# Optimization experiments

Hardware: AMD Instinct MI355X
Metric: run time of the kernel (lower is better)

## Reference

```python
import jax, jax.numpy as jnp
import numpy as np

HIDDEN = 2048
N_HEADS = 16
N_KV_HEADS = 4
HEAD_DIM = HIDDEN // N_HEADS  # 128
FFN = 4096
N_EXPERTS = 8
TOP_K = 2
T = 2048
EPS = 1e-5
ROPE_THETA = 10000.0


def setup_inputs() -> dict:
    key = jax.random.key(0)
    ks = jax.random.split(key, 10)
    s = 0.02
    q_size = N_HEADS * HEAD_DIM
    kv_size = N_KV_HEADS * HEAD_DIM
    return {
        "hidden_states": jax.random.normal(ks[0], (T, HIDDEN), jnp.float32),
        "positions": jnp.arange(T, dtype=jnp.int32),
        "norm1_w": jnp.ones((HIDDEN,), jnp.float32),
        "norm2_w": jnp.ones((HIDDEN,), jnp.float32),
        "wqkv": jax.random.normal(ks[1], (q_size + 2 * kv_size, HIDDEN), jnp.float32) * s,
        "wo": jax.random.normal(ks[2], (HIDDEN, q_size), jnp.float32) * s,
        "gate_w": jax.random.normal(ks[3], (N_EXPERTS, HIDDEN), jnp.float32) * s,
        "w1": jax.random.normal(ks[4], (N_EXPERTS, FFN, HIDDEN), jnp.float32) * s,
        "w2": jax.random.normal(ks[5], (N_EXPERTS, HIDDEN, FFN), jnp.float32) * s,
        "w3": jax.random.normal(ks[6], (N_EXPERTS, FFN, HIDDEN), jnp.float32) * s,
    }


def _rms_norm(x, w):
    var = jnp.mean(x * x, axis=-1, keepdims=True)
    return x * jax.lax.rsqrt(var + EPS) * w


def _rope(x, positions):
    # neox-style rotary: x [T, H, D], split in halves
    half = HEAD_DIM // 2
    inv_freq = 1.0 / (ROPE_THETA ** (jnp.arange(0, half, dtype=jnp.float32) * 2.0 / HEAD_DIM))
    ang = positions.astype(jnp.float32)[:, None] * inv_freq[None, :]  # [T, half]
    cos = jnp.cos(ang)[:, None, :]  # [T, 1, half]
    sin = jnp.sin(ang)[:, None, :]
    x1, x2 = x[..., :half], x[..., half:]
    return jnp.concatenate([x1 * cos - x2 * sin, x2 * cos + x1 * sin], axis=-1)


def reference(hidden_states, positions, norm1_w, norm2_w, wqkv, wo, gate_w, w1, w2, w3):
    q_size = N_HEADS * HEAD_DIM
    kv_size = N_KV_HEADS * HEAD_DIM

    # --- input RMSNorm + attention ---
    residual = hidden_states
    h = _rms_norm(hidden_states, norm1_w)
    qkv = h @ wqkv.T  # [T, q+2kv]
    q = qkv[:, :q_size].reshape(T, N_HEADS, HEAD_DIM)
    k = qkv[:, q_size:q_size + kv_size].reshape(T, N_KV_HEADS, HEAD_DIM)
    v = qkv[:, q_size + kv_size:].reshape(T, N_KV_HEADS, HEAD_DIM)
    q = _rope(q, positions)
    k = _rope(k, positions)
    rep = N_HEADS // N_KV_HEADS
    k = jnp.repeat(k, rep, axis=1)  # [T, H, D]
    v = jnp.repeat(v, rep, axis=1)

    scale = HEAD_DIM ** -0.5
    scores = jnp.einsum('thd,shd->hts', q, k) * scale  # [H, T, T]
    causal = jnp.tril(jnp.ones((T, T), dtype=bool))
    scores = jnp.where(causal[None], scores, jnp.finfo(scores.dtype).min)
    probs = jax.nn.softmax(scores, axis=-1)
    attn = jnp.einsum('hts,shd->thd', probs, v).reshape(T, q_size)
    attn_out = attn @ wo.T

    # --- residual, post-attn RMSNorm ---
    h = attn_out + residual
    residual2 = h
    h = _rms_norm(h, norm2_w)

    # --- MoE: gate -> softmax -> top-k -> renormalize -> SwiGLU experts ---
    logits = h @ gate_w.T  # [T, E]
    routing = jax.nn.softmax(logits.astype(jnp.float32), axis=-1)
    top_vals, top_idx = jax.lax.top_k(routing, TOP_K)  # [T, K]
    top_vals = top_vals / jnp.sum(top_vals, axis=-1, keepdims=True)
    # dense per-token expert weight matrix [T, E] (zero for unselected experts)
    w_full = jnp.zeros((T, N_EXPERTS), jnp.float32).at[
        jnp.arange(T)[:, None], top_idx].add(top_vals)

    h1 = jnp.einsum('td,efd->etf', h, w1)  # [E, T, F]
    h3 = jnp.einsum('td,efd->etf', h, w3)
    g = jax.nn.silu(h1) * h3
    out_e = jnp.einsum('etf,edf->etd', g, w2)  # [E, T, D]
    moe_out = jnp.einsum('etd,te->td', out_e, w_full)

    return moe_out + residual2
```

## Files before the change

### kernel.cpp

```cpp
#include <hip/hip_runtime.h>
#include <math.h>

typedef __fp16 f16;
typedef __fp16 f16x8 __attribute__((ext_vector_type(8)));
typedef __fp16 f16x4 __attribute__((ext_vector_type(4)));
typedef float  f32x4 __attribute__((ext_vector_type(4)));

#define T_SEQ 2048
#define HID   2048
#define NQH   16
#define NKV   4
#define HD    128
#define FFN_D 4096
#define NEXP  8

#define GLDS(gp, lp) __builtin_amdgcn_global_load_lds( \
    (const __attribute__((address_space(1))) void*)(gp), \
    (__attribute__((address_space(3))) void*)(lp), 16, 0, 0)

__device__ __forceinline__ float wredsum(float v){
#pragma unroll
  for (int m = 32; m; m >>= 1) v += __shfl_xor(v, m, 64);
  return v;
}
__device__ __forceinline__ float wredmax(float v){
#pragma unroll
  for (int m = 32; m; m >>= 1) v = fmaxf(v, __shfl_xor(v, m, 64));
  return v;
}

template<bool GATHER_A>
__global__ __launch_bounds__(256, 2)
void gemm_ffn(const f16* __restrict__ A, const f16* __restrict__ B1,
              const f16* __restrict__ B3, f16* __restrict__ G,
              int K, int lda, int ldb, int ldg, long sBz,
              const int* __restrict__ grp_off, const int* __restrict__ a_rows)
{
  __shared__ __align__(16) f16 Lds[2][12288];
  const int bn = blockIdx.x, bm = blockIdx.y, e = blockIdx.z;
  const int rowBase  = grp_off[e];
  const int rowCount = grp_off[e + 1] - rowBase;
  if (rowCount <= 0 || bm * 128 >= rowCount) return;
  const f16* B1z = B1 + (long)e * sBz;
  const f16* B3z = B3 + (long)e * sBz;
  const int nt = K >> 5;

  const int tid = threadIdx.x, lane = tid & 63, w = tid >> 6;
  const int wr = w >> 1, wc = w & 1;

  const int srow = tid >> 2;
  const int scol = (((tid & 3) ^ ((tid >> 3) & 3)) << 3);
  int aoff[2], boff[2];
#pragma unroll
  for (int i = 0; i < 2; i++) {
    int r = bm * 128 + i * 64 + srow;
    if (r > rowCount - 1) r = rowCount - 1;
    const int ar = GATHER_A ? a_rows[rowBase + r] : (rowBase + r);
    aoff[i] = ar * lda + scol;
    boff[i] = (bn * 128 + i * 64 + srow) * ldb + scol;
  }

#define STGF(buf, kk) do { f16* _l = &Lds[buf][0]; \
  GLDS(A   + aoff[0] + (kk), _l +         w * 512); \
  GLDS(A   + aoff[1] + (kk), _l +  2048 + w * 512); \
  GLDS(B1z + boff[0] + (kk), _l +  4096 + w * 512); \
  GLDS(B1z + boff[1] + (kk), _l +  6144 + w * 512); \
  GLDS(B3z + boff[0] + (kk), _l +  8192 + w * 512); \
  GLDS(B3z + boff[1] + (kk), _l + 10240 + w * 512); } while (0)

  const int fr = lane & 15, fq = lane >> 4;
  const int cp = ((fq ^ ((fr >> 1) & 3)) << 3);
  const int aRow  = (wr * 64 + fr) * 32;
  const int b1Row = 4096 + (wc * 64 + fr) * 32;
  const int b3Row = 8192 + (wc * 64 + fr) * 32;

  f32x4 acc1[4][4] = {};
  f32x4 acc3[4][4] = {};

  STGF(0, 0);
  if (nt > 1) STGF(1, 32);

  for (int kt = 0; kt < nt; kt++) {
    if (kt + 1 < nt) asm volatile("s_waitcnt vmcnt(6)" ::: "memory");
    else             asm volatile("s_waitcnt vmcnt(0)" ::: "memory");
    __builtin_amdgcn_s_barrier();
    const f16* Lb = &Lds[kt & 1][0];
    f16x8 af[4], b1f[4], b3f[4];
#pragma unroll
    for (int m = 0; m < 4; m++) af[m]  = *(const f16x8*)(Lb + aRow  + m * 512 + cp);
#pragma unroll
    for (int n = 0; n < 4; n++) b1f[n] = *(const f16x8*)(Lb + b1Row + n * 512 + cp);
#pragma unroll
    for (int n = 0; n < 4; n++) b3f[n] = *(const f16x8*)(Lb + b3Row + n * 512 + cp);
    asm volatile("s_waitcnt lgkmcnt(0)" ::: "memory");
    __builtin_amdgcn_sched_barrier(0);
    __builtin_amdgcn_s_barrier();
    if (kt + 2 < nt) STGF(kt & 1, (kt + 2) * 32);
    __builtin_amdgcn_s_setprio(1);
#pragma unroll
    for (int m = 0; m < 4; m++)
#pragma unroll
      for (int n = 0; n < 4; n++) {
        acc1[m][n] = __builtin_amdgcn_mfma_f32_16x16x32_f16(af[m], b1f[n], acc1[m][n], 0, 0, 0);
        acc3[m][n] = __builtin_amdgcn_mfma_f32_16x16x32_f16(af[m], b3f[n], acc3[m][n], 0, 0, 0);
      }
    __builtin_amdgcn_s_setprio(0);
  }
#undef STGF

  const int ccol0 = bn * 128 + wc * 64 + fr;
#pragma unroll
  for (int m = 0; m < 4; m++) {
#pragma unroll
    for (int r = 0; r < 4; r++) {
      const int g = bm * 128 + wr * 64 + m * 16 + fq * 4 + r;
      if (g >= rowCount) continue;
      const long orow = rowBase + g;
#pragma unroll
      for (int n = 0; n < 4; n++) {
        const float h1 = acc1[m][n][r];
        const float h3 = acc3[m][n][r];
        const float s  = h1 / (1.0f + __expf(-h1));
        G[orow * ldg + (ccol0 + n * 16)] = (f16)(s * h3);
      }
    }
  }
}

template<bool GATHER_A, bool SCATTER_C, int EPI, int MODE>
__global__ __launch_bounds__(256, 4)
void gemm8(const f16* __restrict__ A, const f16* __restrict__ B,
           void* __restrict__ Cv, void* __restrict__ Cv2,
           int K, int lda, int ldb, int ldc, long sBz,
           const int* __restrict__ grp_off, const int* __restrict__ a_rows,
           const int* __restrict__ c_rows, const float* __restrict__ tw)
{
  __shared__ __align__(16) f16 Lds[2][8192];
  const int bn = blockIdx.x, bm = blockIdx.y, z = blockIdx.z;
  int e = z, half = 0;
  if (MODE == 1) { e = z >> 1; half = z & 1; }
  const int rowBase  = grp_off[e];
  const int rowCount = grp_off[e + 1] - rowBase;
  if (rowCount <= 0 || bm * 128 >= rowCount) return;
  const f16* Bz = B + (long)e * sBz;
  int k0 = 0, kN = K;
  if (MODE == 1) { kN = K >> 1; k0 = half * kN; }
  const int nt = kN >> 5;

  const int tid = threadIdx.x, lane = tid & 63, w = tid >> 6;
  const int wr = w >> 1, wc = w & 1;

  const int srow = tid >> 2;
  const int scol = (((tid & 3) ^ ((tid >> 3) & 3)) << 3);
  int aoff[2], boff[2];
#pragma unroll
  for (int i = 0; i < 2; i++) {
    int r = bm * 128 + i * 64 + srow;
    if (r > rowCount - 1) r = rowCount - 1;
    const int ar = GATHER_A ? a_rows[rowBase + r] : (rowBase + r);
    aoff[i] = ar * lda + scol + k0;
    boff[i] = (bn * 128 + i * 64 + srow) * ldb + scol + k0;
  }

#define STG8(buf, kk) do { f16* _l = &Lds[buf][0]; \
  GLDS(A  + aoff[0] + (kk), _l +        w * 512); \
  GLDS(A  + aoff[1] + (kk), _l + 2048 + w * 512); \
  GLDS(Bz + boff[0] + (kk), _l + 4096 + w * 512); \
  GLDS(Bz + boff[1] + (kk), _l + 6144 + w * 512); } while (0)

  const int fr = lane & 15, fq = lane >> 4;
  const int cp = ((fq ^ ((fr >> 1) & 3)) << 3);
  const int aRow = (wr * 64 + fr) * 32;
  const int bRow = 4096 + (wc * 64 + fr) * 32;

  f32x4 acc[4][4] = {};

  STG8(0, 0);
  if (nt > 1) STG8(1, 32);

  for (int kt = 0; kt < nt; kt++) {
    if (kt + 1 < nt) asm volatile("s_waitcnt vmcnt(4)" ::: "memory");
    else             asm volatile("s_waitcnt vmcnt(0)" ::: "memory");
    __builtin_amdgcn_s_barrier();
    const f16* Lb = &Lds[kt & 1][0];
    f16x8 bf[4], af[4];
#pragma unroll
    for (int n = 0; n < 4; n++) bf[n] = *(const f16x8*)(Lb + bRow + n * 512 + cp);
#pragma unroll
    for (int m = 0; m < 4; m++) af[m] = *(const f16x8*)(Lb + aRow + m * 512 + cp);
    asm volatile("s_waitcnt lgkmcnt(0)" ::: "memory");
    __builtin_amdgcn_sched_barrier(0);
    __builtin_amdgcn_s_barrier();
    if (kt + 2 < nt) STG8(kt & 1, (kt + 2) * 32);
    __builtin_amdgcn_s_setprio(1);
#pragma unroll
    for (int m = 0; m < 4; m++)
#pragma unroll
      for (int n = 0; n < 4; n++)
        acc[m][n] = __builtin_amdgcn_mfma_f32_16x16x32_f16(af[m], bf[n], acc[m][n], 0, 0, 0);
    __builtin_amdgcn_s_setprio(0);
  }
#undef STG8

  float* Cf = (MODE == 1 && half) ? (float*)Cv2 : (float*)Cv;
  f16*   Ch = (MODE == 1 && half) ? (f16*)Cv2   : (f16*)Cv;
  const int ccol0 = bn * 128 + wc * 64 + fr;
#pragma unroll
  for (int m = 0; m < 4; m++) {
#pragma unroll
    for (int r = 0; r < 4; r++) {
      const int g = bm * 128 + wr * 64 + m * 16 + fq * 4 + r;
      if (g >= rowCount) continue;
      const long orow = SCATTER_C ? (long)c_rows[rowBase + g] : (long)(rowBase + g);
#pragma unroll
      for (int n = 0; n < 4; n++) {
        const long idx = orow * ldc + (ccol0 + n * 16);
        if (EPI == 4) {
          const int t = (int)(orow & (T_SEQ - 1)), kk = (int)(orow >> 11);
          Ch[idx] = (f16)(tw[t * 2 + kk] * acc[m][n][r]);
        }
        else if (EPI == 3) Ch[idx] = (f16)acc[m][n][r];
        else               Cf[idx] = acc[m][n][r];
      }
    }
  }
}

template<int EPI, int CAUSAL, bool PVK>
__global__ __launch_bounds__(512, 2)
void gemm83(const f16* __restrict__ Ah, const f16* __restrict__ Al,
            const f16* __restrict__ Bh, const f16* __restrict__ Bl,
            void* __restrict__ Cv, int K, int lda, int ldb, int ldc,
            long sAz, long sBz, int bdiv, long sCz,
            const float* __restrict__ resid)
{
  __shared__ __align__(16) f16 Lds[2][32768];
  const int bn = blockIdx.x, bm = blockIdx.y, z = blockIdx.z;
  if (CAUSAL == 1 && bn > bm) return;
  int head = z, chunk = 0;
  if (PVK) { head = z & 7; chunk = z >> 3; }
  int kstart = 0, kend = K;
  if (PVK) {
    const int km = (bm + 1) * 128;
    if (km < kend) kend = km;
    kstart = chunk * 1024;
    if (kstart >= kend) return;
    if (kend > kstart + 1024) kend = kstart + 1024;
  }
  const int nt = (kend - kstart) >> 6;

  const f16* Ahz = Ah + (long)head * sAz;
  const f16* Alz = Al + (long)head * sAz;
  const long zb = (long)(bdiv ? head / bdiv : head) * sBz;
  const f16* Bhz = Bh + zb;
  const f16* Blz = Bl + zb;

  const int tid = threadIdx.x, lane = tid & 63, w = tid >> 6;
  const int wr = w >> 2, wc = w & 3;

  const int srow = w * 8 + (lane >> 3);
  const int scol = (((lane & 7) ^ (lane >> 3)) << 3);
  long ar[2], br[2];
#pragma unroll
  for (int i = 0; i < 2; i++) {
    ar[i] = (long)(bm * 128 + i * 64 + srow) * lda + scol + kstart;
    br[i] = (long)(bn * 128 + i * 64 + srow) * ldb + scol + kstart;
  }

#define STG83(buf, kk) do { f16* _l = &Lds[buf][0]; \
  GLDS(Ahz + ar[0] + (kk), _l +         w * 512); GLDS(Ahz + ar[1] + (kk), _l +  4096 + w * 512); \
  GLDS(Alz + ar[0] + (kk), _l +  8192 + w * 512); GLDS(Alz + ar[1] + (kk), _l + 12288 + w * 512); \
  GLDS(Bhz + br[0] + (kk), _l + 16384 + w * 512); GLDS(Bhz + br[1] + (kk), _l + 20480 + w * 512); \
  GLDS(Blz + br[0] + (kk), _l + 24576 + w * 512); GLDS(Blz + br[1] + (kk), _l + 28672 + w * 512); } while (0)

  const int fr = lane & 15, fq = lane >> 4;
  const int cp0 = ((fq       ^ (fr & 7)) << 3);
  const int cp1 = (((4 | fq) ^ (fr & 7)) << 3);
  const int aRow = (wr * 64 + fr) * 64;
  const int bRow = 16384 + (wc * 32 + fr) * 64;

  f32x4 acc[4][2] = {};

  STG83(0, 0);
  if (nt > 1) STG83(1, 64);

  for (int kt = 0; kt < nt; kt++) {
    if (kt + 1 < nt) asm volatile("s_waitcnt vmcnt(8)" ::: "memory");
    else             asm volatile("s_waitcnt vmcnt(0)" ::: "memory");
    __builtin_amdgcn_s_barrier();
    const f16* Lb = &Lds[kt & 1][0];
#pragma unroll
    for (int ks = 0; ks < 2; ks++) {
      const int cp = ks ? cp1 : cp0;
      f16x8 ah[4], al[4], bh[2], bl[2];
#pragma unroll
      for (int n = 0; n < 2; n++) {
        bh[n] = *(const f16x8*)(Lb + bRow +        n * 1024 + cp);
        bl[n] = *(const f16x8*)(Lb + bRow + 8192 + n * 1024 + cp);
      }
#pragma unroll
      for (int m = 0; m < 4; m++) {
        ah[m] = *(const f16x8*)(Lb + aRow +        m * 1024 + cp);
        al[m] = *(const f16x8*)(Lb + aRow + 8192 + m * 1024 + cp);
      }
      __builtin_amdgcn_s_setprio(1);
#pragma unroll
      for (int m = 0; m < 4; m++)
#pragma unroll
        for (int n = 0; n < 2; n++) {
          acc[m][n] = __builtin_amdgcn_mfma_f32_16x16x32_f16(ah[m], bh[n], acc[m][n], 0, 0, 0);
          acc[m][n] = __builtin_amdgcn_mfma_f32_16x16x32_f16(ah[m], bl[n], acc[m][n], 0, 0, 0);
          acc[m][n] = __builtin_amdgcn_mfma_f32_16x16x32_f16(al[m], bh[n], acc[m][n], 0, 0, 0);
        }
      __builtin_amdgcn_s_setprio(0);
    }
    __builtin_amdgcn_s_barrier();
    if (kt + 2 < nt) STG83(kt & 1, (kt + 2) * 64);
  }
#undef STG83

  float* Cf = (float*)Cv + (long)head * sCz + (PVK ? (long)chunk * T_SEQ * HID : 0);
  const int crow0 = bm * 128 + wr * 64 + fq * 4;
  const int ccol0 = bn * 128 + wc * 32 + fr;
#pragma unroll
  for (int m = 0; m < 4; m++) {
#pragma unroll
    for (int r = 0; r < 4; r++) {
      const long row = crow0 + m * 16 + r;
#pragma unroll
      for (int n = 0; n < 2; n++) {
        const long idx = row * ldc + (ccol0 + n * 16);
        const float v = acc[m][n][r];
        if (EPI == 2) Cf[idx] = v + resid[idx];
        else          Cf[idx] = v;
      }
    }
  }
}

template<bool SPLIT>
__global__ __launch_bounds__(256)
void rmsnorm_k(const float* __restrict__ x, const float* __restrict__ w,
               f16* __restrict__ hi, f16* __restrict__ lo, float* __restrict__ invr_out)
{
  const int t = blockIdx.x, tid = threadIdx.x;
  const float4* xr = (const float4*)(x + (long)t * HID);
  const float4 a = xr[tid * 2], b = xr[tid * 2 + 1];
  float ss = a.x*a.x + a.y*a.y + a.z*a.z + a.w*a.w
           + b.x*b.x + b.y*b.y + b.z*b.z + b.w*b.w;
  ss = wredsum(ss);
  __shared__ float red[4];
  if ((tid & 63) == 0) red[tid >> 6] = ss;
  __syncthreads();
  const float tot  = red[0] + red[1] + red[2] + red[3];
  const float invr = 1.0f / sqrtf(tot * (1.0f / HID) + 1e-5f);
  if (invr_out && tid == 0) invr_out[t] = invr;
  const float4* wr4 = (const float4*)w;
  const float4 wa = wr4[tid * 2], wb = wr4[tid * 2 + 1];
  const float vals[8] = { a.x*wa.x, a.y*wa.y, a.z*wa.z, a.w*wa.w,
                          b.x*wb.x, b.y*wb.y, b.z*wb.z, b.w*wb.w };
  f16x8 hv, lv;
#pragma unroll
  for (int j = 0; j < 8; j++) {
    const float y = vals[j] * invr;
    const f16 h = (f16)y;
    hv[j] = h;
    if (SPLIT) lv[j] = (f16)(y - (float)h);
  }
  const long base = (long)t * HID + tid * 8;
  *(f16x8*)(hi + base) = hv;
  if (SPLIT) *(f16x8*)(lo + base) = lv;
}

__global__ __launch_bounds__(256)
void rope_split_k(const float* __restrict__ qkv, const int* __restrict__ pos,
                  f16* __restrict__ qh, f16* __restrict__ ql,
                  f16* __restrict__ kh, f16* __restrict__ kl,
                  f16* __restrict__ vh, f16* __restrict__ vl)
{
  const int t = blockIdx.x, tid = threadIdx.x;
  __shared__ float invf[64];
  if (tid < 64) {
    const float y = (float)tid * (1.0f / 64.0f);
    invf[tid] = 1.0f / (float)pow(10000.0, (double)y);
  }
  __syncthreads();
  const float p = (float)pos[t];
  const float* row = qkv + (long)t * 3072;

#pragma unroll
  for (int i = 0; i < 4; i++) {
    const int pi = tid + i * 256;
    const int h = pi >> 6, d = pi & 63;
    const float ang = p * invf[d];
    float s, c; sincosf(ang, &s, &c);
    const float x1 = row[h * 128 + d], x2 = row[h * 128 + 64 + d];
    const float o1 = x1 * c - x2 * s;
    const float o2 = x2 * c + x1 * s;
    const long base = ((long)h * T_SEQ + t) * HD;
    { const f16 hh = (f16)o1; qh[base + d]      = hh; ql[base + d]      = (f16)(o1 - (float)hh); }
    { const f16 hh = (f16)o2; qh[base + 64 + d] = hh; ql[base + 64 + d] = (f16)(o2 - (float)hh); }
  }
  {
    const int g = tid >> 6, d = tid & 63;
    const float ang = p * invf[d];
    float s, c; sincosf(ang, &s, &c);
    const float x1 = row[2048 + g * 128 + d], x2 = row[2048 + g * 128 + 64 + d];
    const float o1 = x1 * c - x2 * s;
    const float o2 = x2 * c + x1 * s;
    const long base = ((long)g * T_SEQ + t) * HD;
    { const f16 hh = (f16)o1; kh[base + d]      = hh; kl[base + d]      = (f16)(o1 - (float)hh); }
    { const f16 hh = (f16)o2; kh[base + 64 + d] = hh; kl[base + 64 + d] = (f16)(o2 - (float)hh); }
  }
#pragma unroll
  for (int i = 0; i < 2; i++) {
    const int e = tid + i * 256;
    const int g = e >> 7, d = e & 127;
    const float v = row[2560 + e];
    const long idx = ((long)g * HD + d) * T_SEQ + t;
    const f16 h = (f16)v; vh[idx] = h; vl[idx] = (f16)(v - (float)h);
  }
}

__global__ __launch_bounds__(256)
void softmax_pack(float* __restrict__ S)
{
  const int row  = blockIdx.x * 4 + (threadIdx.x >> 6);
  const int lane = threadIdx.x & 63;
  const int t    = row & (T_SEQ - 1);
  const int nseg = (t >> 8) + 1;
  float* Sr = S + (long)row * T_SEQ;
  float4 v[8];
  const float4* Sr4 = (const float4*)Sr;
#pragma unroll
  for (int i = 0; i < 8; i++) if (i < nseg) v[i] = Sr4[i * 64 + lane];
  const float scale = 0.08838834764831843f;
  float vmax = -3.4e38f;
#pragma unroll
  for (int i = 0; i < 8; i++) {
    if (i >= nseg) continue;
    float* pv = (float*)&v[i];
    const int s0 = (i * 64 + lane) * 4;
#pragma unroll
    for (int j = 0; j < 4; j++) {
      const float xx = (s0 + j <= t) ? pv[j] * scale : -3.4e38f;
      pv[j] = xx;
      vmax = fmaxf(vmax, xx);
    }
  }
  vmax = wredmax(vmax);
  float sum = 0.f;
#pragma unroll
  for (int i = 0; i < 8; i++) {
    if (i >= nseg) continue;
    float* pv = (float*)&v[i];
#pragma unroll
    for (int j = 0; j < 4; j++) {
      const float e = (pv[j] > -3.0e38f) ? __expf(pv[j] - vmax) : 0.f;
      pv[j] = e; sum += e;
    }
  }
  sum = wredsum(sum);
  const float rinv = 1.0f / sum;
  __syncthreads();
  f16* P = (f16*)Sr;
#pragma unroll
  for (int i = 0; i < 8; i++) {
    if (i >= nseg) continue;
    const int s0 = (i * 64 + lane) * 4;
    float* pv = (float*)&v[i];
    f16x4 hv, lv;
#pragma unroll
    for (int j = 0; j < 4; j++) {
      const float pr = pv[j] * rinv;
      const f16 ph = (f16)pr;
      hv[j] = ph; lv[j] = (f16)(pr - (float)ph);
    }
    *(f16x4*)(P + s0)         = hv;
    *(f16x4*)(P + T_SEQ + s0) = lv;
  }
}

__global__ __launch_bounds__(256)
void gate_topk(const float* __restrict__ h2, const float* __restrict__ invr,
               const float* __restrict__ n2w, const float* __restrict__ gw,
               int* __restrict__ top_idx, float* __restrict__ top_w)
{
  const int t = blockIdx.x, tid = threadIdx.x;
  const float r = invr[t];
  const float4* xr = (const float4*)(h2 + (long)t * HID);
  const float4 a = xr[tid * 2], b = xr[tid * 2 + 1];
  const float4* wr4 = (const float4*)n2w;
  const float4 wa = wr4[tid * 2], wb = wr4[tid * 2 + 1];
  const float hn[8] = { a.x*wa.x*r, a.y*wa.y*r, a.z*wa.z*r, a.w*wa.w*r,
                        b.x*wb.x*r, b.y*wb.y*r, b.z*wb.z*r, b.w*wb.w*r };
  float part[8];
#pragma unroll
  for (int e = 0; e < 8; e++) {
    const float4* g4 = (const float4*)(gw + (long)e * HID + tid * 8);
    const float4 ga = g4[0], gb = g4[1];
    part[e] = hn[0]*ga.x + hn[1]*ga.y + hn[2]*ga.z + hn[3]*ga.w
            + hn[4]*gb.x + hn[5]*gb.y + hn[6]*gb.z + hn[7]*gb.w;
  }
#pragma unroll
  for (int e = 0; e < 8; e++) part[e] = wredsum(part[e]);
  __shared__ float red[4][8];
  if ((tid & 63) == 0) {
#pragma unroll
    for (int e = 0; e < 8; e++) red[tid >> 6][e] = part[e];
  }
  __syncthreads();
  if (tid == 0) {
    float lg[8];
#pragma unroll
    for (int e = 0; e < 8; e++) lg[e] = red[0][e] + red[1][e] + red[2][e] + red[3][e];
    int i1 = 0;
    for (int e = 1; e < 8; e++) if (lg[e] > lg[i1]) i1 = e;
    int i2 = -1;
    for (int e = 0; e < 8; e++) { if (e == i1) continue; if (i2 < 0 || lg[e] > lg[i2]) i2 = e; }
    const float q = expf(lg[i2] - lg[i1]);
    top_idx[t * 2] = i1; top_idx[t * 2 + 1] = i2;
    top_w[t * 2]     = 1.0f / (1.0f + q);
    top_w[t * 2 + 1] = q / (1.0f + q);
  }
}

__global__ __launch_bounds__(256)
void route_build(const int* __restrict__ ti, int* __restrict__ goff,
                 int* __restrict__ arows, int* __restrict__ crows)
{
  __shared__ int cnt[8], cur[8], off[9];
  const int tid = threadIdx.x;
  if (tid < 8) { cnt[tid] = 0; cur[tid] = 0; }
  __syncthreads();
  for (int i = tid; i < 2 * T_SEQ; i += 256) atomicAdd(&cnt[ti[i]], 1);
  __syncthreads();
  if (tid == 0) {
    int s = 0;
    for (int e = 0; e < NEXP; e++) { off[e] = s; s += cnt[e]; }
    off[NEXP] = s;
    for (int e = 0; e <= NEXP; e++) goff[e] = off[e];
  }
  __syncthreads();
  for (int i = tid; i < 2 * T_SEQ; i += 256) {
    const int e = ti[i];
    const int p = atomicAdd(&cur[e], 1);
    const int slot = off[e] + p;
    arows[slot] = i >> 1;
    crows[slot] = (i & 1) * T_SEQ + (i >> 1);
  }
}

__global__ __launch_bounds__(256)
void split_pair_k(const float* __restrict__ src, f16* __restrict__ hi, f16* __restrict__ lo)
{
  const long i = ((long)blockIdx.x * 256 + threadIdx.x) * 8;
  const float4 a = *(const float4*)(src + i);
  const float4 b = *(const float4*)(src + i + 4);
  const float vals[8] = {a.x,a.y,a.z,a.w,b.x,b.y,b.z,b.w};
  f16x8 hv, lv;
#pragma unroll
  for (int j = 0; j < 8; j++) { const f16 h = (f16)vals[j]; hv[j] = h; lv[j] = (f16)(vals[j] - (float)h); }
  *(f16x8*)(hi + i) = hv;
  *(f16x8*)(lo + i) = lv;
}

__global__ __launch_bounds__(256)
void split_sum_k(const float* __restrict__ c0, const float* __restrict__ c1,
                 f16* __restrict__ hi, f16* __restrict__ lo)
{
  const long i = ((long)blockIdx.x * 256 + threadIdx.x) * 8;
  const int t = (int)(i >> 11);
  const float4 a = *(const float4*)(c0 + i);
  const float4 b = *(const float4*)(c0 + i + 4);
  float4 ca = {0,0,0,0}, cb = {0,0,0,0};
  if (t >= 1024) { ca = *(const float4*)(c1 + i); cb = *(const float4*)(c1 + i + 4); }
  const float vals[8] = {a.x+ca.x, a.y+ca.y, a.z+ca.z, a.w+ca.w,
                         b.x+cb.x, b.y+cb.y, b.z+cb.z, b.w+cb.w};
  f16x8 hv, lv;
#pragma unroll
  for (int j = 0; j < 8; j++) { const f16 h = (f16)vals[j]; hv[j] = h; lv[j] = (f16)(vals[j] - (float)h); }
  *(f16x8*)(hi + i) = hv;
  *(f16x8*)(lo + i) = lv;
}

__global__ __launch_bounds__(256)
void conv_f16_k(const float* __restrict__ src, f16* __restrict__ dst)
{
  const long i = ((long)blockIdx.x * 256 + threadIdx.x) * 8;
  const float4 a = *(const float4*)(src + i);
  const float4 b = *(const float4*)(src + i + 4);
  f16x8 o;
  o[0]=(f16)a.x; o[1]=(f16)a.y; o[2]=(f16)a.z; o[3]=(f16)a.w;
  o[4]=(f16)b.x; o[5]=(f16)b.y; o[6]=(f16)b.z; o[7]=(f16)b.w;
  *(f16x8*)(dst + i) = o;
}

__global__ __launch_bounds__(256)
void combine_k(const float* __restrict__ h2, const f16* __restrict__ c0,
               const f16* __restrict__ c1, float* __restrict__ out)
{
  const long i = ((long)blockIdx.x * 256 + threadIdx.x) * 4;
  const float4 a = *(const float4*)(h2 + i);
  const f16x4 p0 = *(const f16x4*)(c0 + i);
  const f16x4 p1 = *(const f16x4*)(c1 + i);
  const f16x4 q0 = *(const f16x4*)(c0 + (long)T_SEQ * HID + i);
  const f16x4 q1 = *(const f16x4*)(c1 + (long)T_SEQ * HID + i);
  float4 o;
  o.x = a.x + (float)p0[0] + (float)p1[0] + (float)q0[0] + (float)q1[0];
  o.y = a.y + (float)p0[1] + (float)p1[1] + (float)q0[1] + (float)q1[1];
  o.z = a.z + (float)p0[2] + (float)p1[2] + (float)q0[2] + (float)q1[2];
  o.w = a.w + (float)p0[3] + (float)p1[3] + (float)q0[3] + (float)q1[3];
  *(float4*)(out + i) = o;
}

extern "C" void kernel_launch(void* const* d_in, const int* in_sizes, int n_in,
                              void* d_out, int out_size, void* d_ws, size_t ws_size,
                              hipStream_t stream)
{
  const float* x    = (const float*)d_in[0];
  const int*   pos  = (const int*)d_in[1];
  const float* n1w  = (const float*)d_in[2];
  const float* n2w  = (const float*)d_in[3];
  const float* wqkv = (const float*)d_in[4];
  const float* wo   = (const float*)d_in[5];
  const float* gw   = (const float*)d_in[6];
  const float* w1   = (const float*)d_in[7];
  const float* w2   = (const float*)d_in[8];
  const float* w3   = (const float*)d_in[9];
  float* out = (float*)d_out;

  char* base = (char*)d_ws;
  size_t off = 0;
  auto alloc = [&](size_t bytes) -> char* {
    char* r = base + off;
    off += (bytes + 255) & ~(size_t)255;
    return r;
  };
  f16* w1h = (f16*)alloc((size_t)NEXP * FFN_D * HID * 2);
  f16* w3h = (f16*)alloc((size_t)NEXP * FFN_D * HID * 2);
  f16* w2h = (f16*)alloc((size_t)NEXP * FFN_D * HID * 2);
  f16* wqh = (f16*)alloc((size_t)3072 * HID * 2);
  f16* wql = (f16*)alloc((size_t)3072 * HID * 2);
  f16* woh = (f16*)alloc((size_t)HID * HID * 2);
  f16* wol = (f16*)alloc((size_t)HID * HID * 2);
  f16* qh  = (f16*)alloc((size_t)NQH * T_SEQ * HD * 2);
  f16* ql  = (f16*)alloc((size_t)NQH * T_SEQ * HD * 2);
  f16* kh  = (f16*)alloc((size_t)NKV * T_SEQ * HD * 2);
  f16* kl  = (f16*)alloc((size_t)NKV * T_SEQ * HD * 2);
  f16* vh  = (f16*)alloc((size_t)NKV * T_SEQ * HD * 2);
  f16* vl  = (f16*)alloc((size_t)NKV * T_SEQ * HD * 2);
  float* h2      = (float*)alloc((size_t)T_SEQ * HID * 4);
  f16*   h2n     = (f16*)alloc((size_t)T_SEQ * HID * 2);
  float* contrib = (float*)alloc((size_t)2 * T_SEQ * HID * 4);
  float* invr2 = (float*)alloc(T_SEQ * 4);
  int*   tidx  = (int*)alloc(T_SEQ * 2 * 4);
  float* twt   = (float*)alloc(T_SEQ * 2 * 4);
  int*   counts = (int*)alloc(256);
  int*   goff   = (int*)alloc(256);
  int*   arows  = (int*)alloc(2 * T_SEQ * 4);
  int*   crows  = (int*)alloc(2 * T_SEQ * 4);
  (void)counts;
  char* uA = alloc((size_t)T_SEQ * 3072 * 4);
  float* qkvf = (float*)uA;
  char* uB = alloc((size_t)T_SEQ * HID * 2);
  f16* hh = (f16*)uB; f16* ahh = (f16*)uB;
  char* uC = alloc((size_t)T_SEQ * HID * 2);
  f16* hl = (f16*)uC; f16* ahl = (f16*)uC;
  char* uS = alloc((size_t)8 * T_SEQ * T_SEQ * 4);
  float* Sbuf = (float*)uS;
  f16* gb  = (f16*)(uS + (size_t)4 * T_SEQ * FFN_D * 2);
  f16* contribH = (f16*)(uS + (size_t)6 * T_SEQ * FFN_D * 2);

  if (off > ws_size) return;

  conv_f16_k<<<(NEXP * FFN_D * HID) / (256 * 8), 256, 0, stream>>>(w1, w1h);
  conv_f16_k<<<(NEXP * FFN_D * HID) / (256 * 8), 256, 0, stream>>>(w3, w3h);
  conv_f16_k<<<(NEXP * FFN_D * HID) / (256 * 8), 256, 0, stream>>>(w2, w2h);
  split_pair_k<<<(3072 * HID) / (256 * 8), 256, 0, stream>>>(wqkv, wqh, wql);
  split_pair_k<<<(HID * HID) / (256 * 8), 256, 0, stream>>>(wo, woh, wol);

  rmsnorm_k<true><<<T_SEQ, 256, 0, stream>>>(x, n1w, hh, hl, nullptr);
  gemm83<0,0,false><<<dim3(3072/128, T_SEQ/128, 1), 512, 0, stream>>>(
      hh, hl, wqh, wql, qkvf, HID, HID, HID, 3072, 0, 0, 0, 0, nullptr);
  rope_split_k<<<T_SEQ, 256, 0, stream>>>(qkvf, pos, qh, ql, kh, kl, vh, vl);

  for (int grp = 0; grp < 2; grp++) {
    const f16* qh_g = qh + (size_t)grp * 8 * T_SEQ * HD;
    const f16* ql_g = ql + (size_t)grp * 8 * T_SEQ * HD;
    const f16* kh_g = kh + (size_t)grp * 2 * T_SEQ * HD;
    const f16* kl_g = kl + (size_t)grp * 2 * T_SEQ * HD;
    const f16* vh_g = vh + (size_t)grp * 2 * HD * T_SEQ;
    const f16* vl_g = vl + (size_t)grp * 2 * HD * T_SEQ;
    float* attn_g = contrib + (size_t)grp * 8 * HD;
    gemm83<0,1,false><<<dim3(T_SEQ/128, T_SEQ/128, 8), 512, 0, stream>>>(
        qh_g, ql_g, kh_g, kl_g, Sbuf, HD, HD, HD, T_SEQ,
        (long)T_SEQ * HD, (long)T_SEQ * HD, 4, (long)T_SEQ * T_SEQ, nullptr);
    softmax_pack<<<8 * T_SEQ / 4, 256, 0, stream>>>(Sbuf);
    gemm83<0,0,true><<<dim3(1, T_SEQ/128, 16), 512, 0, stream>>>(
        (const f16*)Sbuf, (const f16*)Sbuf + T_SEQ, vh_g, vl_g, attn_g,
        T_SEQ, 2 * T_SEQ, T_SEQ, HID,
        (long)T_SEQ * 2 * T_SEQ, (long)HD * T_SEQ, 4, HD, nullptr);
  }

  split_sum_k<<<(T_SEQ * HID) / (256 * 8), 256, 0, stream>>>(contrib, contrib + (size_t)T_SEQ * HID, ahh, ahl);
  gemm83<2,0,false><<<dim3(HID/128, T_SEQ/128, 1), 512, 0, stream>>>(
      ahh, ahl, woh, wol, h2, HID, HID, HID, HID, 0, 0, 0, 0, x);

  rmsnorm_k<false><<<T_SEQ, 256, 0, stream>>>(h2, n2w, h2n, nullptr, invr2);
  gate_topk<<<T_SEQ, 256, 0, stream>>>(h2, invr2, n2w, gw, tidx, twt);
  route_build<<<1, 256, 0, stream>>>(tidx, goff, arows, crows);

  gemm_ffn<true><<<dim3(FFN_D/128, 16, NEXP), 256, 0, stream>>>(
      h2n, w1h, w3h, gb, HID, HID, HID, FFN_D, (long)FFN_D * HID, goff, arows);
  gemm8<false,true,4,1><<<dim3(HID/128, 16, 2 * NEXP), 256, 0, stream>>>(
      gb, w2h, contrib, contribH, FFN_D, FFN_D, FFN_D, HID, (long)HID * FFN_D,
      goff, nullptr, crows, twt);
  combine_k<<<(T_SEQ * HID) / (256 * 4), 256, 0, stream>>>(h2, (const f16*)contrib, contribH, out);
}
```

Before: 936.9 us.

## Fuse fp32-to-fp16 expert weight conversion into MoE GEMM tile loads

Drops the three standalone kernels that converted w1, w3 and w2 to fp16 before every call. The expert GEMMs now stage fp32 weight tiles directly into LDS with a new swizzle and convert to fp16 in registers just before the MFMAs. This removes a large full-weight read/write pass over the expert weights. In exchange, each GEMM tile reads twice the weight bytes from global memory, possibly repeatedly across row tiles. LDS use per block also grows, and the gemm8 occupancy hint drops from 4 to 3.

```diff
diff --git a/kernel.cpp b/kernel.cpp
--- a/kernel.cpp
+++ b/kernel.cpp
@@ -31,48 +31,59 @@
 
 template<bool GATHER_A>
 __global__ __launch_bounds__(256, 2)
-void gemm_ffn(const f16* __restrict__ A, const f16* __restrict__ B1,
-              const f16* __restrict__ B3, f16* __restrict__ G,
+void gemm_ffn(const f16* __restrict__ A, const float* __restrict__ B1,
+              const float* __restrict__ B3, f16* __restrict__ G,
               int K, int lda, int ldb, int ldg, long sBz,
               const int* __restrict__ grp_off, const int* __restrict__ a_rows)
 {
-  __shared__ __align__(16) f16 Lds[2][12288];
+  __shared__ __align__(16) f16 Lds[2][20480];
   const int bn = blockIdx.x, bm = blockIdx.y, e = blockIdx.z;
   const int rowBase  = grp_off[e];
   const int rowCount = grp_off[e + 1] - rowBase;
   if (rowCount <= 0 || bm * 128 >= rowCount) return;
-  const f16* B1z = B1 + (long)e * sBz;
-  const f16* B3z = B3 + (long)e * sBz;
+  const float* B1z = B1 + (long)e * sBz;
+  const float* B3z = B3 + (long)e * sBz;
   const int nt = K >> 5;
 
   const int tid = threadIdx.x, lane = tid & 63, w = tid >> 6;
   const int wr = w >> 1, wc = w & 1;
 
-  const int srow = tid >> 2;
-  const int scol = (((tid & 3) ^ ((tid >> 3) & 3)) << 3);
-  int aoff[2], boff[2];
+  const int sArow = tid >> 2;
+  const int sAcol = (((tid & 3) ^ ((tid >> 3) & 3)) << 3);
+  int aoff[2];
 #pragma unroll
   for (int i = 0; i < 2; i++) {
-    int r = bm * 128 + i * 64 + srow;
+    int r = bm * 128 + i * 64 + sArow;
     if (r > rowCount - 1) r = rowCount - 1;
     const int ar = GATHER_A ? a_rows[rowBase + r] : (rowBase + r);
-    aoff[i] = ar * lda + scol;
-    boff[i] = (bn * 128 + i * 64 + srow) * ldb + scol;
-  }
+    aoff[i] = ar * lda + sAcol;
+  }
+  const int sBrow = tid >> 3;
+  const int sBcol = (((tid & 7) ^ ((tid >> 3) & 7)) << 2);
+  int boff[4];
+#pragma unroll
+  for (int i = 0; i < 4; i++)
+    boff[i] = (bn * 128 + i * 32 + sBrow) * ldb + sBcol;
 
 #define STGF(buf, kk) do { f16* _l = &Lds[buf][0]; \
-  GLDS(A   + aoff[0] + (kk), _l +         w * 512); \
-  GLDS(A   + aoff[1] + (kk), _l +  2048 + w * 512); \
-  GLDS(B1z + boff[0] + (kk), _l +  4096 + w * 512); \
-  GLDS(B1z + boff[1] + (kk), _l +  6144 + w * 512); \
-  GLDS(B3z + boff[0] + (kk), _l +  8192 + w * 512); \
-  GLDS(B3z + boff[1] + (kk), _l + 10240 + w * 512); } while (0)
+  float* _b1 = (float*)(_l + 4096); float* _b3 = (float*)(_l + 12288); \
+  GLDS(A   + aoff[0] + (kk), _l +        w * 512); \
+  GLDS(A   + aoff[1] + (kk), _l + 2048 + w * 512); \
+  GLDS(B1z + boff[0] + (kk), _b1 +        w * 256); \
+  GLDS(B1z + boff[1] + (kk), _b1 + 1024 + w * 256); \
+  GLDS(B1z + boff[2] + (kk), _b1 + 2048 + w * 256); \
+  GLDS(B1z + boff[3] + (kk), _b1 + 3072 + w * 256); \
+  GLDS(B3z + boff[0] + (kk), _b3 +        w * 256); \
+  GLDS(B3z + boff[1] + (kk), _b3 + 1024 + w * 256); \
+  GLDS(B3z + boff[2] + (kk), _b3 + 2048 + w * 256); \
+  GLDS(B3z + boff[3] + (kk), _b3 + 3072 + w * 256); } while (0)
 
   const int fr = lane & 15, fq = lane >> 4;
-  const int cp = ((fq ^ ((fr >> 1) & 3)) << 3);
-  const int aRow  = (wr * 64 + fr) * 32;
-  const int b1Row = 4096 + (wc * 64 + fr) * 32;
-  const int b3Row = 8192 + (wc * 64 + fr) * 32;
+  const int cpA  = ((fq ^ ((fr >> 1) & 3)) << 3);
+  const int aRow = (wr * 64 + fr) * 32;
+  const int gB0  = (((2 * fq)     ^ (fr & 7)) << 2);
+  const int gB1  = (((2 * fq + 1) ^ (fr & 7)) << 2);
+  const int bRowF = (wc * 64 + fr) * 32;
 
   f32x4 acc1[4][4] = {};
   f32x4 acc3[4][4] = {};
@@ -81,17 +92,26 @@
   if (nt > 1) STGF(1, 32);
 
   for (int kt = 0; kt < nt; kt++) {
-    if (kt + 1 < nt) asm volatile("s_waitcnt vmcnt(6)" ::: "memory");
+    if (kt + 1 < nt) asm volatile("s_waitcnt vmcnt(10)" ::: "memory");
     else             asm volatile("s_waitcnt vmcnt(0)" ::: "memory");
     __builtin_amdgcn_s_barrier();
     const f16* Lb = &Lds[kt & 1][0];
+    const float* B1b = (const float*)(Lb + 4096);
+    const float* B3b = (const float*)(Lb + 12288);
     f16x8 af[4], b1f[4], b3f[4];
 #pragma unroll
-    for (int m = 0; m < 4; m++) af[m]  = *(const f16x8*)(Lb + aRow  + m * 512 + cp);
-#pragma unroll
-    for (int n = 0; n < 4; n++) b1f[n] = *(const f16x8*)(Lb + b1Row + n * 512 + cp);
-#pragma unroll
-    for (int n = 0; n < 4; n++) b3f[n] = *(const f16x8*)(Lb + b3Row + n * 512 + cp);
+    for (int m = 0; m < 4; m++) af[m] = *(const f16x8*)(Lb + aRow + m * 512 + cpA);
+#pragma unroll
+    for (int n = 0; n < 4; n++) {
+      const float4 u1 = *(const float4*)(B1b + bRowF + n * 512 + gB0);
+      const float4 v1 = *(const float4*)(B1b + bRowF + n * 512 + gB1);
+      const float4 u3 = *(const float4*)(B3b + bRowF + n * 512 + gB0);
+      const float4 v3 = *(const float4*)(B3b + bRowF + n * 512 + gB1);
+      b1f[n][0]=(f16)u1.x; b1f[n][1]=(f16)u1.y; b1f[n][2]=(f16)u1.z; b1f[n][3]=(f16)u1.w;
+      b1f[n][4]=(f16)v1.x; b1f[n][5]=(f16)v1.y; b1f[n][6]=(f16)v1.z; b1f[n][7]=(f16)v1.w;
+      b3f[n][0]=(f16)u3.x; b3f[n][1]=(f16)u3.y; b3f[n][2]=(f16)u3.z; b3f[n][3]=(f16)u3.w;
+      b3f[n][4]=(f16)v3.x; b3f[n][5]=(f16)v3.y; b3f[n][6]=(f16)v3.z; b3f[n][7]=(f16)v3.w;
+    }
     asm volatile("s_waitcnt lgkmcnt(0)" ::: "memory");
     __builtin_amdgcn_sched_barrier(0);
     __builtin_amdgcn_s_barrier();
@@ -128,21 +148,21 @@
 }
 
 template<bool GATHER_A, bool SCATTER_C, int EPI, int MODE>
-__global__ __launch_bounds__(256, 4)
-void gemm8(const f16* __restrict__ A, const f16* __restrict__ B,
+__global__ __launch_bounds__(256, 3)
+void gemm8(const f16* __restrict__ A, const float* __restrict__ B,
            void* __restrict__ Cv, void* __restrict__ Cv2,
            int K, int lda, int ldb, int ldc, long sBz,
            const int* __restrict__ grp_off, const int* __restrict__ a_rows,
            const int* __restrict__ c_rows, const float* __restrict__ tw)
 {
-  __shared__ __align__(16) f16 Lds[2][8192];
+  __shared__ __align__(16) f16 Lds[2][12288];
   const int bn = blockIdx.x, bm = blockIdx.y, z = blockIdx.z;
   int e = z, half = 0;
   if (MODE == 1) { e = z >> 1; half = z & 1; }
   const int rowBase  = grp_off[e];
   const int rowCount = grp_off[e + 1] - rowBase;
   if (rowCount <= 0 || bm * 128 >= rowCount) return;
-  const f16* Bz = B + (long)e * sBz;
+  const float* Bz = B + (long)e * sBz;
   int k0 = 0, kN = K;
   if (MODE == 1) { kN = K >> 1; k0 = half * kN; }
   const int nt = kN >> 5;
@@ -150,28 +170,38 @@
   const int tid = threadIdx.x, lane = tid & 63, w = tid >> 6;
   const int wr = w >> 1, wc = w & 1;
 
-  const int srow = tid >> 2;
-  const int scol = (((tid & 3) ^ ((tid >> 3) & 3)) << 3);
-  int aoff[2], boff[2];
+  const int sArow = tid >> 2;
+  const int sAcol = (((tid & 3) ^ ((tid >> 3) & 3)) << 3);
+  int aoff[2];
 #pragma unroll
   for (int i = 0; i < 2; i++) {
-    int r = bm * 128 + i * 64 + srow;
+    int r = bm * 128 + i * 64 + sArow;
     if (r > rowCount - 1) r = rowCount - 1;
     const int ar = GATHER_A ? a_rows[rowBase + r] : (rowBase + r);
-    aoff[i] = ar * lda + scol + k0;
-    boff[i] = (bn * 128 + i * 64 + srow) * ldb + scol + k0;
-  }
+    aoff[i] = ar * lda + sAcol + k0;
+  }
+  const int sBrow = tid >> 3;
+  const int sBcol = (((tid & 7) ^ ((tid >> 3) & 7)) << 2);
+  int boff[4];
+#pragma unroll
+  for (int i = 0; i < 4; i++)
+    boff[i] = (bn * 128 + i * 32 + sBrow) * ldb + sBcol + k0;
 
 #define STG8(buf, kk) do { f16* _l = &Lds[buf][0]; \
+  float* _b = (float*)(_l + 4096); \
   GLDS(A  + aoff[0] + (kk), _l +        w * 512); \
   GLDS(A  + aoff[1] + (kk), _l + 2048 + w * 512); \
-  GLDS(Bz + boff[0] + (kk), _l + 4096 + w * 512); \
-  GLDS(Bz + boff[1] + (kk), _l + 6144 + w * 512); } while (0)
+  GLDS(Bz + boff[0] + (kk), _b +        w * 256); \
+  GLDS(Bz + boff[1] + (kk), _b + 1024 + w * 256); \
+  GLDS(Bz + boff[2] + (kk), _b + 2048 + w * 256); \
+  GLDS(Bz + boff[3] + (kk), _b + 3072 + w * 256); } while (0)
 
   const int fr = lane & 15, fq = lane >> 4;
-  const int cp = ((fq ^ ((fr >> 1) & 3)) << 3);
+  const int cpA  = ((fq ^ ((fr >> 1) & 3)) << 3);
   const int aRow = (wr * 64 + fr) * 32;
-  const int bRow = 4096 + (wc * 64 + fr) * 32;
+  const int gB0  = (((2 * fq)     ^ (fr & 7)) << 2);
+  const int gB1  = (((2 * fq + 1) ^ (fr & 7)) << 2);
+  const int bRowF = (wc * 64 + fr) * 32;
 
   f32x4 acc[4][4] = {};
 
@@ -179,15 +209,21 @@
   if (nt > 1) STG8(1, 32);
 
   for (int kt = 0; kt < nt; kt++) {
-    if (kt + 1 < nt) asm volatile("s_waitcnt vmcnt(4)" ::: "memory");
+    if (kt + 1 < nt) asm volatile("s_waitcnt vmcnt(6)" ::: "memory");
     else             asm volatile("s_waitcnt vmcnt(0)" ::: "memory");
     __builtin_amdgcn_s_barrier();
     const f16* Lb = &Lds[kt & 1][0];
-    f16x8 bf[4], af[4];
-#pragma unroll
-    for (int n = 0; n < 4; n++) bf[n] = *(const f16x8*)(Lb + bRow + n * 512 + cp);
-#pragma unroll
-    for (int m = 0; m < 4; m++) af[m] = *(const f16x8*)(Lb + aRow + m * 512 + cp);
+    const float* Bb = (const float*)(Lb + 4096);
+    f16x8 af[4], bf[4];
+#pragma unroll
+    for (int m = 0; m < 4; m++) af[m] = *(const f16x8*)(Lb + aRow + m * 512 + cpA);
+#pragma unroll
+    for (int n = 0; n < 4; n++) {
+      const float4 u = *(const float4*)(Bb + bRowF + n * 512 + gB0);
+      const float4 v = *(const float4*)(Bb + bRowF + n * 512 + gB1);
+      bf[n][0]=(f16)u.x; bf[n][1]=(f16)u.y; bf[n][2]=(f16)u.z; bf[n][3]=(f16)u.w;
+      bf[n][4]=(f16)v.x; bf[n][5]=(f16)v.y; bf[n][6]=(f16)v.z; bf[n][7]=(f16)v.w;
+    }
     asm volatile("s_waitcnt lgkmcnt(0)" ::: "memory");
     __builtin_amdgcn_sched_barrier(0);
     __builtin_amdgcn_s_barrier();
@@ -585,18 +621,6 @@
 }
 
 __global__ __launch_bounds__(256)
-void conv_f16_k(const float* __restrict__ src, f16* __restrict__ dst)
-{
-  const long i = ((long)blockIdx.x * 256 + threadIdx.x) * 8;
-  const float4 a = *(const float4*)(src + i);
-  const float4 b = *(const float4*)(src + i + 4);
-  f16x8 o;
-  o[0]=(f16)a.x; o[1]=(f16)a.y; o[2]=(f16)a.z; o[3]=(f16)a.w;
-  o[4]=(f16)b.x; o[5]=(f16)b.y; o[6]=(f16)b.z; o[7]=(f16)b.w;
-  *(f16x8*)(dst + i) = o;
-}
-
-__global__ __launch_bounds__(256)
 void combine_k(const float* __restrict__ h2, const f16* __restrict__ c0,
                const f16* __restrict__ c1, float* __restrict__ out)
 {
@@ -637,9 +661,6 @@
     off += (bytes + 255) & ~(size_t)255;
     return r;
   };
-  f16* w1h = (f16*)alloc((size_t)NEXP * FFN_D * HID * 2);
-  f16* w3h = (f16*)alloc((size_t)NEXP * FFN_D * HID * 2);
-  f16* w2h = (f16*)alloc((size_t)NEXP * FFN_D * HID * 2);
   f16* wqh = (f16*)alloc((size_t)3072 * HID * 2);
   f16* wql = (f16*)alloc((size_t)3072 * HID * 2);
   f16* woh = (f16*)alloc((size_t)HID * HID * 2);
@@ -656,11 +677,9 @@
   float* invr2 = (float*)alloc(T_SEQ * 4);
   int*   tidx  = (int*)alloc(T_SEQ * 2 * 4);
   float* twt   = (float*)alloc(T_SEQ * 2 * 4);
-  int*   counts = (int*)alloc(256);
   int*   goff   = (int*)alloc(256);
   int*   arows  = (int*)alloc(2 * T_SEQ * 4);
   int*   crows  = (int*)alloc(2 * T_SEQ * 4);
-  (void)counts;
   char* uA = alloc((size_t)T_SEQ * 3072 * 4);
   float* qkvf = (float*)uA;
   char* uB = alloc((size_t)T_SEQ * HID * 2);
@@ -674,9 +693,6 @@
 
   if (off > ws_size) return;
 
-  conv_f16_k<<<(NEXP * FFN_D * HID) / (256 * 8), 256, 0, stream>>>(w1, w1h);
-  conv_f16_k<<<(NEXP * FFN_D * HID) / (256 * 8), 256, 0, stream>>>(w3, w3h);
-  conv_f16_k<<<(NEXP * FFN_D * HID) / (256 * 8), 256, 0, stream>>>(w2, w2h);
   split_pair_k<<<(3072 * HID) / (256 * 8), 256, 0, stream>>>(wqkv, wqh, wql);
   split_pair_k<<<(HID * HID) / (256 * 8), 256, 0, stream>>>(wo, woh, wol);
 
@@ -712,9 +728,9 @@
   route_build<<<1, 256, 0, stream>>>(tidx, goff, arows, crows);
 
   gemm_ffn<true><<<dim3(FFN_D/128, 16, NEXP), 256, 0, stream>>>(
-      h2n, w1h, w3h, gb, HID, HID, HID, FFN_D, (long)FFN_D * HID, goff, arows);
+      h2n, w1, w3, gb, HID, HID, HID, FFN_D, (long)FFN_D * HID, goff, arows);
   gemm8<false,true,4,1><<<dim3(HID/128, 16, 2 * NEXP), 256, 0, stream>>>(
-      gb, w2h, contrib, contribH, FFN_D, FFN_D, FFN_D, HID, (long)HID * FFN_D,
+      gb, w2, contrib, contribH, FFN_D, FFN_D, FFN_D, HID, (long)HID * FFN_D,
       goff, nullptr, crows, twt);
   combine_k<<<(T_SEQ * HID) / (256 * 4), 256, 0, stream>>>(h2, (const f16*)contrib, contribH, out);
 }
```

Measured after the change: 855.5 us. 8.7% less time.
